# Kernel optimization log

Measured on AMD Instinct MI355X. Metric: run time of the kernel, lower is better.

Reference implementation:

```python
import jax, jax.numpy as jnp
import numpy as np

B, T, D, H = 8, 2048, 2048, 128  # batch, seq_len, d_model, head_size
NEG = -1e9


def setup_inputs() -> dict:
    key = jax.random.key(0)
    k0, k1, k2, k3 = jax.random.split(key, 4)
    x = jax.random.normal(k0, (B, T, D), dtype=jnp.float32)
    s = 1.0 / np.sqrt(D)
    Wq = jax.random.normal(k1, (D, H), dtype=jnp.float32) * s
    Wk = jax.random.normal(k2, (D, H), dtype=jnp.float32) * s
    Wv = jax.random.normal(k3, (D, H), dtype=jnp.float32) * s
    return {"x": x, "Wq": Wq, "Wk": Wk, "Wv": Wv}


def reference(x, Wq, Wk, Wv):
    # projections: [B,T,H]
    q = jnp.einsum('btd,dh->bth', x, Wq)
    k = jnp.einsum('btd,dh->bth', x, Wk)
    v = jnp.einsum('btd,dh->bth', x, Wv)
    # NOTE: module multiplies by sqrt(head_size) (faithful to source)
    wei = jnp.einsum('bqh,bkh->bqk', q, k) * jnp.sqrt(jnp.float32(H))
    causal = jnp.tril(jnp.ones((T, T), dtype=bool))
    wei = jnp.where(causal, wei, jnp.float32(NEG))
    wei = jax.nn.softmax(wei, axis=-1)
    # dropout is identity (deterministic=True / rate=0)
    out = jnp.einsum('bqk,bkh->bqh', wei, v)
    return out
```

## Files before the change

kernel.cpp:

```cpp
#include <hip/hip_runtime.h>
#include <math.h>

#define B_ 8
#define T_ 2048
#define D_ 2048
#define H_ 128
#define M_ (B_ * T_)

typedef __bf16 bf16x8 __attribute__((ext_vector_type(8)));
typedef __bf16 bf16x4 __attribute__((ext_vector_type(4)));
typedef float f32x4 __attribute__((ext_vector_type(4)));

#define MFMA(a, b, c) __builtin_amdgcn_mfma_f32_16x16x32_bf16(a, b, c, 0, 0, 0)

#define QH_OFF 0
#define QL_OFF (1 * 2097152)
#define KH_OFF (2 * 2097152)
#define KL_OFF (3 * 2097152)
#define VT_OFF (4 * 2097152)
#define WTH_OFF (5 * 2097152)
#define WTL_OFF (WTH_OFF + 786432)

#define GL_LDS16(gp, lp)                                      \
  __builtin_amdgcn_global_load_lds(                           \
      (const __attribute__((address_space(1))) void*)(gp),    \
      (__attribute__((address_space(3))) void*)(lp), 16, 0, 0)

__global__ __launch_bounds__(256) void prep_kernel(
    const float* __restrict__ Wq, const float* __restrict__ Wk,
    const float* __restrict__ Wv, __bf16* __restrict__ wpk_hi,
    __bf16* __restrict__ wpk_lo) {
  const int z = blockIdx.y;
  const int k0 = blockIdx.x * 64;
  const float* W = z == 0 ? Wq : z == 1 ? Wk : Wv;
  __shared__ float tile[64][132];
  const int t = threadIdx.x;
#pragma unroll
  for (int it = 0; it < 8; ++it) {
    int f4 = it * 256 + t;
    int row = f4 >> 5, c = (f4 & 31) << 2;
    *(float4*)&tile[row][c] = *(const float4*)&W[(size_t)(k0 + row) * H_ + c];
  }
  __syncthreads();
  int n = t >> 1, kh = (t & 1) << 5;
  __bf16 h[32], l[32];
#pragma unroll
  for (int kk = 0; kk < 32; ++kk) {
    float x = tile[kh + kk][n];
    __bf16 hi = (__bf16)x;
    h[kk] = hi;
    l[kk] = (__bf16)(x - (float)hi);
  }
  const int nf = z * H_ + n;
  const int g = nf >> 4, l15 = nf & 15;
  const int s = (k0 + kh) >> 5;
#pragma unroll
  for (int c = 0; c < 4; ++c) {
    size_t dst = ((size_t)(g * 64 + s) * 64 + c * 16 + l15) * 8;
    *(bf16x8*)&wpk_hi[dst] = *(bf16x8*)&h[c * 8];
    *(bf16x8*)&wpk_lo[dst] = *(bf16x8*)&l[c * 8];
  }
}

#define XSTR 72

#define XCONV(RW, NB)                                                       \
  {                                                                         \
    __bf16 h0 = (__bf16)RW.x, h1 = (__bf16)RW.y, h2 = (__bf16)RW.z,         \
           h3 = (__bf16)RW.w;                                               \
    bf16x4 hv = {h0, h1, h2, h3};                                           \
    bf16x4 lv = {(__bf16)(RW.x - (float)h0), (__bf16)(RW.y - (float)h1),    \
                 (__bf16)(RW.z - (float)h2), (__bf16)(RW.w - (float)h3)};   \
    *(bf16x4*)&Xs[NB][xm * XSTR + xk] = hv;                                 \
    *(bf16x4*)&Xs[NB][xm * XSTR + 32 + xk] = lv;                            \
  }

#define COMPUTE(CUR)                                                        \
  {                                                                         \
    bf16x8 ah[2], al[2];                                                    \
    _Pragma("unroll") for (int mg = 0; mg < 2; ++mg) {                      \
      ah[mg] = *(bf16x8*)&Xs[CUR][(wr * 32 + mg * 16 + l15) * XSTR + q8];   \
      al[mg] =                                                              \
          *(bf16x8*)&Xs[CUR][(wr * 32 + mg * 16 + l15) * XSTR + 32 + q8];   \
    }                                                                       \
    _Pragma("unroll") for (int nt = 0; nt < 3; ++nt) {                      \
      const int g = wc * 3 + nt;                                            \
      bf16x8 bh = *(bf16x8*)&Wf[CUR][g * 512 + lane * 8];                   \
      bf16x8 bl = *(bf16x8*)&Wf[CUR][6144 + g * 512 + lane * 8];            \
      _Pragma("unroll") for (int mg = 0; mg < 2; ++mg) {                    \
        acc[mg][nt] = MFMA(ah[mg], bh, acc[mg][nt]);                        \
        acc[mg][nt] = MFMA(al[mg], bh, acc[mg][nt]);                        \
        acc[mg][nt] = MFMA(ah[mg], bl, acc[mg][nt]);                        \
      }                                                                     \
    }                                                                       \
  }

#define PSTEP(KS, RW, RL)                                                   \
  {                                                                         \
    const int nb_ = ((KS)&1) ^ 1;                                           \
    _Pragma("unroll") for (int i = 0; i < 3; ++i)                           \
        GL_LDS16(gsrc[i] + ((KS) + 1) * 512, ldst0[i] + nb_ * 12288);       \
    __builtin_amdgcn_sched_barrier(0);        \
    RL = *(const float4*)(xgp + ((KS) + 2) * 32);                           \
    XCONV(RW, nb_);                                                         \
    COMPUTE((KS)&1);                                                        \
    asm volatile("s_waitcnt vmcnt(1) lgkmcnt(0)" ::: "memory");             \
    __builtin_amdgcn_sched_barrier(0);                                      \
    __builtin_amdgcn_s_barrier();                                           \
    __builtin_amdgcn_sched_barrier(0);                                      \
  }

__global__ __launch_bounds__(512, 4) void proj_kernel(
    const float* __restrict__ X, const __bf16* __restrict__ wpk_hi,
    const __bf16* __restrict__ wpk_lo, __bf16* __restrict__ qh,
    __bf16* __restrict__ ql, __bf16* __restrict__ kh,
    __bf16* __restrict__ kl, __bf16* __restrict__ vt) {
  __shared__ __align__(16) __bf16 Wf[2][12288];
  __shared__ __align__(16) __bf16 Xs[2][64 * XSTR];
  const int t = threadIdx.x;
  const int wv = t >> 6, lane = t & 63;
  const int l15 = lane & 15, quad = lane >> 4, q8 = quad * 8;
  const int bi = blockIdx.x;
  const int m0 = (bi >> 1) * 64;
  const int nbase = (bi & 1) * 192;
  const int wr = wv >> 2, wc = wv & 3;
  const int xm = t >> 3, xk = (t & 7) << 2;
  const float* xgp = X + (size_t)(m0 + xm) * D_ + xk;
  const __bf16* gsrc[3];
  __bf16* ldst0[3];
#pragma unroll
  for (int i = 0; i < 3; ++i) {
    int f = wv * 3 + i;
    int sel = f >= 12;
    int gl = f - sel * 12;
    int gg = (nbase >> 4) + gl;
    gsrc[i] = (sel ? wpk_lo : wpk_hi) + (size_t)gg * 32768 + (size_t)lane * 8;
    ldst0[i] = &Wf[0][sel * 6144 + gl * 512];
  }
  f32x4 acc[2][3] = {};
  {
    float4 x0 = *(const float4*)xgp;
#pragma unroll
    for (int i = 0; i < 3; ++i) GL_LDS16(gsrc[i], ldst0[i]);
    XCONV(x0, 0);
  }
  float4 xA = *(const float4*)(xgp + 32);
  float4 xB;
  asm volatile("s_waitcnt vmcnt(0) lgkmcnt(0)" ::: "memory");
  __builtin_amdgcn_sched_barrier(0);
  __builtin_amdgcn_s_barrier();
  __builtin_amdgcn_sched_barrier(0);
  for (int ks2 = 0; ks2 < 62; ks2 += 2) {
    PSTEP(ks2, xA, xB);
    PSTEP(ks2 + 1, xB, xA);
  }
  {
#pragma unroll
    for (int i = 0; i < 3; ++i)
      GL_LDS16(gsrc[i] + 63 * 512, ldst0[i] + 12288);
    XCONV(xA, 1);
    COMPUTE(0);
    asm volatile("s_waitcnt vmcnt(0) lgkmcnt(0)" ::: "memory");
    __builtin_amdgcn_sched_barrier(0);
    __builtin_amdgcn_s_barrier();
    __builtin_amdgcn_sched_barrier(0);
  }
  COMPUTE(1);
#pragma unroll
  for (int nt = 0; nt < 3; ++nt) {
    int ncb = nbase + wc * 48 + nt * 16;
    int z = ncb >> 7;
    int h = (ncb & 127) + l15;
#pragma unroll
    for (int mg = 0; mg < 2; ++mg) {
      int r0 = m0 + wr * 32 + mg * 16 + quad * 4;
      if (z == 2) {
        int b = m0 >> 11;
        int tt0 = (m0 & 2047) + wr * 32 + mg * 16 + quad * 4;
        bf16x4 pv = {(__bf16)acc[mg][nt][0], (__bf16)acc[mg][nt][1],
                     (__bf16)acc[mg][nt][2], (__bf16)acc[mg][nt][3]};
        *(bf16x4*)&vt[(size_t)(b * H_ + h) * T_ + tt0] = pv;
      } else {
        __bf16* dh = z == 0 ? qh : kh;
        __bf16* dl = z == 0 ? ql : kl;
#pragma unroll
        for (int reg = 0; reg < 4; ++reg) {
          float v = acc[mg][nt][reg];
          __bf16 hi = (__bf16)v;
          dh[(size_t)(r0 + reg) * H_ + h] = hi;
          dl[(size_t)(r0 + reg) * H_ + h] = (__bf16)(v - (float)hi);
        }
      }
    }
  }
}

__global__ __launch_bounds__(512, 1) void attn_kernel(
    const __bf16* __restrict__ qh, const __bf16* __restrict__ qlo,
    const __bf16* __restrict__ kh, const __bf16* __restrict__ klo,
    const __bf16* __restrict__ vt, float* __restrict__ out) {
  const int t = threadIdx.x;
  const int wv = t >> 6, st = wv >> 2, cw = wv & 3;
  const int lane = t & 63, l15 = lane & 15, quad = lane >> 4;
  const int j = blockIdx.x, b = j & 7, pi = j >> 3;
  const int qlidx = (st == 0) ? pi : 63 - pi;
  const int t0 = qlidx * 32;
  const int nkt = (qlidx >> 1) + 1;
  __shared__ __align__(16) __bf16 Pbuf[8][32 * 72];
  __shared__ __align__(16) float Obuf[2][32 * 132];
  __shared__ float mlb[2][4][32], llb[2][4][32];
  const size_t qrow0 = (size_t)b * T_ + t0;
  bf16x8 qfh[2][4], qfl[2][4];
#pragma unroll
  for (int mg = 0; mg < 2; ++mg)
#pragma unroll
    for (int ds = 0; ds < 4; ++ds) {
      size_t off = (qrow0 + mg * 16 + l15) * H_ + ds * 32 + quad * 8;
      qfh[mg][ds] = *(const bf16x8*)(qh + off);
      qfl[mg][ds] = *(const bf16x8*)(qlo + off);
    }
  f32x4 O[2][8] = {};
  float ms[2][4], ls[2][4];
#pragma unroll
  for (int mg = 0; mg < 2; ++mg)
#pragma unroll
    for (int reg = 0; reg < 4; ++reg) {
      ms[mg][reg] = -INFINITY;
      ls[mg][reg] = 0.f;
    }
  const __bf16* vtb = vt + (size_t)b * H_ * T_;
  const float scale = 11.313708498984761f;
  for (int kt_i = cw; kt_i < nkt; kt_i += 4) {
    const int kt = kt_i * 64;
    f32x4 S[2][4] = {};
#pragma unroll
    for (int ds = 0; ds < 4; ++ds)
#pragma unroll
      for (int ct = 0; ct < 4; ++ct) {
        size_t koff =
            ((size_t)b * T_ + kt + ct * 16 + l15) * H_ + ds * 32 + quad * 8;
        bf16x8 bh = *(const bf16x8*)(kh + koff);
        bf16x8 bl = *(const bf16x8*)(klo + koff);
#pragma unroll
        for (int mg = 0; mg < 2; ++mg) {
          S[mg][ct] = MFMA(qfh[mg][ds], bh, S[mg][ct]);
          S[mg][ct] = MFMA(qfl[mg][ds], bh, S[mg][ct]);
          S[mg][ct] = MFMA(qfh[mg][ds], bl, S[mg][ct]);
        }
      }
    const bool diag = (kt_i == nkt - 1);
#pragma unroll
    for (int mg = 0; mg < 2; ++mg)
#pragma unroll
      for (int ct = 0; ct < 4; ++ct)
#pragma unroll
        for (int reg = 0; reg < 4; ++reg) {
          float s = S[mg][ct][reg] * scale;
          if (diag && (kt + ct * 16 + l15 > t0 + mg * 16 + quad * 4 + reg))
            s = -1e30f;
          S[mg][ct][reg] = s;
        }
    float al_[2][4];
#pragma unroll
    for (int mg = 0; mg < 2; ++mg)
#pragma unroll
      for (int reg = 0; reg < 4; ++reg) {
        float r = fmaxf(fmaxf(S[mg][0][reg], S[mg][1][reg]),
                        fmaxf(S[mg][2][reg], S[mg][3][reg]));
        r = fmaxf(r, __shfl_xor(r, 1));
        r = fmaxf(r, __shfl_xor(r, 2));
        r = fmaxf(r, __shfl_xor(r, 4));
        r = fmaxf(r, __shfl_xor(r, 8));
        float mn = fmaxf(ms[mg][reg], r);
        float a = __expf(ms[mg][reg] - mn);
        ms[mg][reg] = mn;
        float ps = 0.f;
#pragma unroll
        for (int ct = 0; ct < 4; ++ct) {
          float p = __expf(S[mg][ct][reg] - mn);
          S[mg][ct][reg] = p;
          ps += p;
        }
        ps += __shfl_xor(ps, 1);
        ps += __shfl_xor(ps, 2);
        ps += __shfl_xor(ps, 4);
        ps += __shfl_xor(ps, 8);
        ls[mg][reg] = ls[mg][reg] * a + ps;
        al_[mg][reg] = a;
      }
#pragma unroll
    for (int mg = 0; mg < 2; ++mg)
#pragma unroll
      for (int ht = 0; ht < 8; ++ht)
#pragma unroll
        for (int reg = 0; reg < 4; ++reg) O[mg][ht][reg] *= al_[mg][reg];
#pragma unroll
    for (int mg = 0; mg < 2; ++mg)
#pragma unroll
      for (int ct = 0; ct < 4; ++ct)
#pragma unroll
        for (int reg = 0; reg < 4; ++reg)
          Pbuf[wv][(mg * 16 + quad * 4 + reg) * 72 + ct * 16 + l15] =
              (__bf16)S[mg][ct][reg];
#pragma unroll
    for (int ks = 0; ks < 2; ++ks) {
      bf16x8 pf0 = *(bf16x8*)&Pbuf[wv][(l15)*72 + ks * 32 + quad * 8];
      bf16x8 pf1 = *(bf16x8*)&Pbuf[wv][(16 + l15) * 72 + ks * 32 + quad * 8];
#pragma unroll
      for (int ht = 0; ht < 8; ++ht) {
        bf16x8 vf = *(const bf16x8*)&vtb[(size_t)(ht * 16 + l15) * T_ + kt +
                                         ks * 32 + quad * 8];
        O[0][ht] = MFMA(pf0, vf, O[0][ht]);
        O[1][ht] = MFMA(pf1, vf, O[1][ht]);
      }
    }
  }
  if (l15 == 0) {
#pragma unroll
    for (int mg = 0; mg < 2; ++mg)
#pragma unroll
      for (int reg = 0; reg < 4; ++reg) {
        mlb[st][cw][mg * 16 + quad * 4 + reg] = ms[mg][reg];
        llb[st][cw][mg * 16 + quad * 4 + reg] = ls[mg][reg];
      }
  }
  for (int i = t; i < 2 * 32 * 132; i += 512) ((float*)Obuf)[i] = 0.f;
  __syncthreads();
  float aw[2][4];
#pragma unroll
  for (int mg = 0; mg < 2; ++mg)
#pragma unroll
    for (int reg = 0; reg < 4; ++reg) {
      int row = mg * 16 + quad * 4 + reg;
      float M = fmaxf(fmaxf(mlb[st][0][row], mlb[st][1][row]),
                      fmaxf(mlb[st][2][row], mlb[st][3][row]));
      float L = 0.f;
#pragma unroll
      for (int w = 0; w < 4; ++w)
        L += llb[st][w][row] * __expf(mlb[st][w][row] - M);
      aw[mg][reg] = __expf(ms[mg][reg] - M) / L;
    }
#pragma unroll
  for (int mg = 0; mg < 2; ++mg)
#pragma unroll
    for (int ht = 0; ht < 8; ++ht)
#pragma unroll
      for (int reg = 0; reg < 4; ++reg)
        atomicAdd(&Obuf[st][(mg * 16 + quad * 4 + reg) * 132 + ht * 16 + l15],
                  O[mg][ht][reg] * aw[mg][reg]);
  __syncthreads();
  {
    const int stw = t >> 8, tt = t & 255;
    const int qlw = (stw == 0) ? pi : 63 - pi;
    const size_t obase = ((size_t)b * T_ + qlw * 32) * H_;
#pragma unroll
    for (int i = 0; i < 4; ++i) {
      int f4 = i * 256 + tt;
      int row = f4 >> 5, c = (f4 & 31) << 2;
      *(float4*)&out[obase + (size_t)row * H_ + c] =
          *(float4*)&Obuf[stw][row * 132 + c];
    }
  }
}

extern "C" void kernel_launch(void* const* d_in, const int* in_sizes, int n_in,
                              void* d_out, int out_size, void* d_ws, size_t ws_size,
                              hipStream_t stream) {
  const float* x = (const float*)d_in[0];
  const float* Wq = (const float*)d_in[1];
  const float* Wk = (const float*)d_in[2];
  const float* Wv = (const float*)d_in[3];
  __bf16* ws = (__bf16*)d_ws;
  float* out = (float*)d_out;
  prep_kernel<<<dim3(32, 3), 256, 0, stream>>>(Wq, Wk, Wv, ws + WTH_OFF,
                                               ws + WTL_OFF);
  proj_kernel<<<512, 512, 0, stream>>>(x, ws + WTH_OFF, ws + WTL_OFF,
                                       ws + QH_OFF, ws + QL_OFF, ws + KH_OFF,
                                       ws + KL_OFF, ws + VT_OFF);
  attn_kernel<<<256, 512, 0, stream>>>(ws + QH_OFF, ws + QL_OFF, ws + KH_OFF,
                                       ws + KL_OFF, ws + VT_OFF, out);
}
```

Baseline: 363.4 us.

## Store Q/K/V projections in MFMA-fragment-packed layout for contiguous attention loads

The projection kernel now writes Q, K (hi/lo bf16 splits) and V^T into a layout where each 16x32 MFMA operand fragment is stored as 64 contiguous lanes of 8 bf16 values. The attention kernel then loads each fragment with one fully coalesced 1 KiB access per wavefront instead of row-strided loads spanning 16 rows. This is meant to cut memory transactions and cache-line waste on the K and V streaming in the inner loop. In exchange, the projection kernel's scalar stores become more scattered, which may slow the epilogue.

```diff
diff --git a/kernel.cpp b/kernel.cpp
--- a/kernel.cpp
+++ b/kernel.cpp
@@ -112,9 +112,9 @@
 
 __global__ __launch_bounds__(512, 4) void proj_kernel(
     const float* __restrict__ X, const __bf16* __restrict__ wpk_hi,
-    const __bf16* __restrict__ wpk_lo, __bf16* __restrict__ qh,
-    __bf16* __restrict__ ql, __bf16* __restrict__ kh,
-    __bf16* __restrict__ kl, __bf16* __restrict__ vt) {
+    const __bf16* __restrict__ wpk_lo, __bf16* __restrict__ qph,
+    __bf16* __restrict__ qpl, __bf16* __restrict__ kph,
+    __bf16* __restrict__ kpl, __bf16* __restrict__ vtp) {
   __shared__ __align__(16) __bf16 Wf[2][12288];
   __shared__ __align__(16) __bf16 Xs[2][64 * XSTR];
   const int t = threadIdx.x;
@@ -174,21 +174,28 @@
 #pragma unroll
     for (int mg = 0; mg < 2; ++mg) {
       int r0 = m0 + wr * 32 + mg * 16 + quad * 4;
+      int b = r0 >> 11;
+      int rr = r0 & 2047;
       if (z == 2) {
-        int b = m0 >> 11;
-        int tt0 = (m0 & 2047) + wr * 32 + mg * 16 + quad * 4;
         bf16x4 pv = {(__bf16)acc[mg][nt][0], (__bf16)acc[mg][nt][1],
                      (__bf16)acc[mg][nt][2], (__bf16)acc[mg][nt][3]};
-        *(bf16x4*)&vt[(size_t)(b * H_ + h) * T_ + tt0] = pv;
+        size_t vi = (((size_t)(b * 64 + (rr >> 5)) * 8 + (h >> 4)) * 64 +
+                     ((rr & 31) >> 3) * 16 + (h & 15)) * 8 + (rr & 7);
+        *(bf16x4*)&vtp[vi] = pv;
       } else {
-        __bf16* dh = z == 0 ? qh : kh;
-        __bf16* dl = z == 0 ? ql : kl;
+        __bf16* dh = z == 0 ? qph : kph;
+        __bf16* dl = z == 0 ? qpl : kpl;
+        int g = rr >> 4;
+        size_t base =
+            (((size_t)(b * 128 + g) * 4 + (h >> 5)) * 64 + ((h & 31) >> 3) * 16)
+                * 8 + (h & 7);
 #pragma unroll
         for (int reg = 0; reg < 4; ++reg) {
           float v = acc[mg][nt][reg];
           __bf16 hi = (__bf16)v;
-          dh[(size_t)(r0 + reg) * H_ + h] = hi;
-          dl[(size_t)(r0 + reg) * H_ + h] = (__bf16)(v - (float)hi);
+          size_t ii = base + (size_t)(quad * 4 + reg) * 8;
+          dh[ii] = hi;
+          dl[ii] = (__bf16)(v - (float)hi);
         }
       }
     }
@@ -196,9 +203,9 @@
 }
 
 __global__ __launch_bounds__(512, 1) void attn_kernel(
-    const __bf16* __restrict__ qh, const __bf16* __restrict__ qlo,
-    const __bf16* __restrict__ kh, const __bf16* __restrict__ klo,
-    const __bf16* __restrict__ vt, float* __restrict__ out) {
+    const __bf16* __restrict__ qph, const __bf16* __restrict__ qpl,
+    const __bf16* __restrict__ kph, const __bf16* __restrict__ kpl,
+    const __bf16* __restrict__ vtp, float* __restrict__ out) {
   const int t = threadIdx.x;
   const int wv = t >> 6, st = wv >> 2, cw = wv & 3;
   const int lane = t & 63, l15 = lane & 15, quad = lane >> 4;
@@ -209,15 +216,15 @@
   __shared__ __align__(16) __bf16 Pbuf[8][32 * 72];
   __shared__ __align__(16) float Obuf[2][32 * 132];
   __shared__ float mlb[2][4][32], llb[2][4][32];
-  const size_t qrow0 = (size_t)b * T_ + t0;
   bf16x8 qfh[2][4], qfl[2][4];
 #pragma unroll
   for (int mg = 0; mg < 2; ++mg)
 #pragma unroll
     for (int ds = 0; ds < 4; ++ds) {
-      size_t off = (qrow0 + mg * 16 + l15) * H_ + ds * 32 + quad * 8;
-      qfh[mg][ds] = *(const bf16x8*)(qh + off);
-      qfl[mg][ds] = *(const bf16x8*)(qlo + off);
+      size_t off =
+          (((size_t)(b * 128 + qlidx * 2 + mg) * 4 + ds) << 9) + lane * 8;
+      qfh[mg][ds] = *(const bf16x8*)(qph + off);
+      qfl[mg][ds] = *(const bf16x8*)(qpl + off);
     }
   f32x4 O[2][8] = {};
   float ms[2][4], ls[2][4];
@@ -228,19 +235,18 @@
       ms[mg][reg] = -INFINITY;
       ls[mg][reg] = 0.f;
     }
-  const __bf16* vtb = vt + (size_t)b * H_ * T_;
   const float scale = 11.313708498984761f;
   for (int kt_i = cw; kt_i < nkt; kt_i += 4) {
     const int kt = kt_i * 64;
     f32x4 S[2][4] = {};
+    const size_t kgb = (size_t)(b * 128 + (kt >> 4));
 #pragma unroll
     for (int ds = 0; ds < 4; ++ds)
 #pragma unroll
       for (int ct = 0; ct < 4; ++ct) {
-        size_t koff =
-            ((size_t)b * T_ + kt + ct * 16 + l15) * H_ + ds * 32 + quad * 8;
-        bf16x8 bh = *(const bf16x8*)(kh + koff);
-        bf16x8 bl = *(const bf16x8*)(klo + koff);
+        size_t kidx = (((kgb + ct) * 4 + ds) << 9) + lane * 8;
+        bf16x8 bh = *(const bf16x8*)(kph + kidx);
+        bf16x8 bl = *(const bf16x8*)(kpl + kidx);
 #pragma unroll
         for (int mg = 0; mg < 2; ++mg) {
           S[mg][ct] = MFMA(qfh[mg][ds], bh, S[mg][ct]);
@@ -306,10 +312,10 @@
     for (int ks = 0; ks < 2; ++ks) {
       bf16x8 pf0 = *(bf16x8*)&Pbuf[wv][(l15)*72 + ks * 32 + quad * 8];
       bf16x8 pf1 = *(bf16x8*)&Pbuf[wv][(16 + l15) * 72 + ks * 32 + quad * 8];
+      const size_t vb = ((size_t)(b * 64 + (kt >> 5) + ks)) << 12;
 #pragma unroll
       for (int ht = 0; ht < 8; ++ht) {
-        bf16x8 vf = *(const bf16x8*)&vtb[(size_t)(ht * 16 + l15) * T_ + kt +
-                                         ks * 32 + quad * 8];
+        bf16x8 vf = *(const bf16x8*)&vtp[vb + (ht << 9) + lane * 8];
         O[0][ht] = MFMA(pf0, vf, O[0][ht]);
         O[1][ht] = MFMA(pf1, vf, O[1][ht]);
       }
```

After: 388.1 us. 1.07x slower.
